# Optimization experiments

Measured on AMD Instinct MI355X. Metric: run time of the kernel, lower is better.

The kernel has to match this reference:

```python
import jax, jax.numpy as jnp
import numpy as np

N = 10000
D_IN = 512
D_OUT = 512
EDGE_P = 0.003  # ~30 avg degree


def setup_inputs() -> dict:
    key = jax.random.key(0)
    k_x, k_a, k_w1, k_b1, k_w2, k_b2 = jax.random.split(key, 6)
    x = jax.random.normal(k_x, (N, D_IN), dtype=jnp.float32)
    # sparse-ish binary adjacency, zero diagonal (GCNConv adds self-loops itself)
    adjacency = (jax.random.uniform(k_a, (N, N)) < EDGE_P).astype(jnp.float32)
    adjacency = adjacency * (1.0 - jnp.eye(N, dtype=jnp.float32))
    s1 = 1.0 / np.sqrt(D_IN)
    s2 = 1.0 / np.sqrt(D_OUT)
    W1 = jax.random.normal(k_w1, (D_IN, D_OUT), dtype=jnp.float32) * s1
    b1 = jax.random.normal(k_b1, (D_OUT,), dtype=jnp.float32) * 0.01
    W2 = jax.random.normal(k_w2, (D_OUT, D_OUT), dtype=jnp.float32) * s2
    b2 = jax.random.normal(k_b2, (D_OUT,), dtype=jnp.float32) * 0.01
    return {"x": x, "adjacency": adjacency, "W1": W1, "b1": b1, "W2": W2, "b2": b2}


def _gcn_norm(adjacency):
    # GCNConv gcn_norm: add self-loops (weight 1), deg = sum of incoming edge
    # weights at target (column sums), norm[i,j] = d_i^{-1/2} * Ahat[i,j] * d_j^{-1/2}
    n = adjacency.shape[0]
    Ahat = adjacency + jnp.eye(n, dtype=adjacency.dtype)
    deg = Ahat.sum(axis=0)
    dinv = jnp.where(deg > 0, deg ** -0.5, 0.0)
    return dinv[:, None] * Ahat * dinv[None, :]


def reference(x, adjacency, W1, b1, W2, b2):
    An = _gcn_norm(adjacency)  # [N, N]
    # out[j] = sum_i An[i,j] * (x W)[i]  ->  An.T @ (x W)
    h = jax.nn.relu(An.T @ (x @ W1) + b1)
    h = jax.nn.relu(An.T @ (h @ W2) + b2)
    return h
```

## Files before the change

kernel.cpp:

```cpp
#include <hip/hip_runtime.h>
#include <hip/hip_bf16.h>
#include <hip/hip_fp16.h>

#define N_NODES 10000
#define DFEAT 512
#define MPAD 10112
#define MAXDEG 96
#define NB_SPLITX 5056
#define NB_WSPLIT 512
#define GEMM_BLOCKS 316
#define NB_SCAN 10000

typedef __attribute__((ext_vector_type(8))) short short8x;
typedef __attribute__((ext_vector_type(4))) float f32x4;
typedef __attribute__((ext_vector_type(4))) _Float16 half4x;

__device__ __forceinline__ ushort f2bf(float f) {
    uint u = __builtin_bit_cast(uint, f);
    uint r = (u + 0x7FFFu + ((u >> 16) & 1u)) >> 16;
    return (ushort)r;
}
__device__ __forceinline__ float bf2f(ushort h) {
    uint u = ((uint)h) << 16;
    return __builtin_bit_cast(float, u);
}

typedef const __attribute__((address_space(1))) void gv_t;
typedef __attribute__((address_space(3))) void sv_t;
__device__ __forceinline__ void gload16(const void* g, void* l) {
    __builtin_amdgcn_global_load_lds((gv_t*)g, (sv_t*)l, 16, 0, 0);
}

__global__ __launch_bounds__(256) void prep_split(const float* __restrict__ X,
                                                  const float* __restrict__ W1,
                                                  const float* __restrict__ W2,
                                                  ushort* __restrict__ Ah,
                                                  ushort* __restrict__ Al,
                                                  ushort* __restrict__ W1hT,
                                                  ushort* __restrict__ W1lT,
                                                  ushort* __restrict__ W2hT,
                                                  ushort* __restrict__ W2lT) {
    const int bid = blockIdx.x;
    const int tid = threadIdx.x;
    if (bid < NB_SPLITX) {
        size_t idx = (size_t)bid * 256 + tid;
        int row = (int)(idx >> 7);
        float4 v = make_float4(0.f, 0.f, 0.f, 0.f);
        if (row < N_NODES) v = ((const float4*)X)[idx];
        ushort4 hi, lo;
        hi.x = f2bf(v.x); lo.x = f2bf(v.x - bf2f(hi.x));
        hi.y = f2bf(v.y); lo.y = f2bf(v.y - bf2f(hi.y));
        hi.z = f2bf(v.z); lo.z = f2bf(v.z - bf2f(hi.z));
        hi.w = f2bf(v.w); lo.w = f2bf(v.w - bf2f(hi.w));
        ((ushort4*)Ah)[idx] = hi;
        ((ushort4*)Al)[idx] = lo;
    } else {
        __shared__ float tile[32][33];
        int wb = bid - NB_SPLITX;
        const float* W = (wb < 256) ? W1 : W2;
        ushort* WhT = (wb < 256) ? W1hT : W2hT;
        ushort* WlT = (wb < 256) ? W1lT : W2lT;
        int wi = wb & 255;
        int n0 = (wi & 15) * 32, k0 = (wi >> 4) * 32;
        const int tx = tid & 31, ty = tid >> 5;
#pragma unroll
        for (int p = 0; p < 4; ++p)
            tile[ty + p * 8][tx] = W[(size_t)(k0 + ty + p * 8) * DFEAT + n0 + tx];
        __syncthreads();
#pragma unroll
        for (int p = 0; p < 4; ++p) {
            int n = n0 + ty + p * 8;
            int k = k0 + tx;
            float v = tile[tx][ty + p * 8];
            ushort h = f2bf(v);
            WhT[(size_t)n * DFEAT + k] = h;
            WlT[(size_t)n * DFEAT + k] = f2bf(v - bf2f(h));
        }
    }
}

template <bool PRE>
__device__ __forceinline__ void gemm_tile(const ushort* __restrict__ Ah,
                                          const ushort* __restrict__ Al,
                                          const ushort* __restrict__ BhT,
                                          const ushort* __restrict__ BlT,
                                          const int* __restrict__ cnt,
                                          _Float16* __restrict__ C, int M,
                                          int row0, int col0, int tid) {
    __shared__ ushort lAh[128 * 32];
    __shared__ ushort lAl[128 * 32];
    __shared__ ushort lBh[128 * 32];
    __shared__ ushort lBl[128 * 32];
    const int lane = tid & 63, wv = tid >> 6;
    const int wm = wv >> 1, wn = wv & 1;
    const int l15 = lane & 15, lg = lane >> 4;

    f32x4 acc[4][4];
#pragma unroll
    for (int i = 0; i < 4; ++i)
#pragma unroll
        for (int j = 0; j < 4; ++j) acc[i][j] = (f32x4){0.f, 0.f, 0.f, 0.f};

    for (int k0 = 0; k0 < 512; k0 += 32) {
#pragma unroll
        for (int c = 0; c < 2; ++c) {
            int o = (wv * 2 + c) * 1024 + lane * 16;
            int r = o >> 6;
            int gsl = ((o >> 4) & 3) ^ (r & 3);
            size_t ga = (size_t)(row0 + r) * 1024 + (size_t)(k0 * 2) + gsl * 16;
            size_t gb = (size_t)(col0 + r) * 1024 + (size_t)(k0 * 2) + gsl * 16;
            gload16((const char*)Ah + ga, (char*)lAh + o);
            gload16((const char*)Al + ga, (char*)lAl + o);
            gload16((const char*)BhT + gb, (char*)lBh + o);
            gload16((const char*)BlT + gb, (char*)lBl + o);
        }
        __syncthreads();

        short8x a_h[4], a_l[4], b_h[4], b_l[4];
#pragma unroll
        for (int i = 0; i < 4; ++i) {
            int r = wm * 64 + i * 16 + l15;
            int bo = r * 64 + ((lg ^ (r & 3)) << 4);
            a_h[i] = *(const short8x*)((const char*)lAh + bo);
            a_l[i] = *(const short8x*)((const char*)lAl + bo);
        }
#pragma unroll
        for (int j = 0; j < 4; ++j) {
            int n = wn * 64 + j * 16 + l15;
            int bo = n * 64 + ((lg ^ (n & 3)) << 4);
            b_h[j] = *(const short8x*)((const char*)lBh + bo);
            b_l[j] = *(const short8x*)((const char*)lBl + bo);
        }
#pragma unroll
        for (int i = 0; i < 4; ++i)
#pragma unroll
            for (int j = 0; j < 4; ++j) {
                acc[i][j] = __builtin_amdgcn_mfma_f32_16x16x32_bf16(a_h[i], b_h[j], acc[i][j], 0, 0, 0);
                acc[i][j] = __builtin_amdgcn_mfma_f32_16x16x32_bf16(a_h[i], b_l[j], acc[i][j], 0, 0, 0);
                acc[i][j] = __builtin_amdgcn_mfma_f32_16x16x32_bf16(a_l[i], b_h[j], acc[i][j], 0, 0, 0);
            }
        __syncthreads();
    }

#pragma unroll
    for (int i = 0; i < 4; ++i) {
#pragma unroll
        for (int r = 0; r < 4; ++r) {
            int grow = row0 + wm * 64 + i * 16 + lg * 4 + r;
            if (grow < M) {
                float dv = 1.0f;
                if (PRE) dv = 1.0f / sqrtf((float)cnt[grow] + 1.0f);
#pragma unroll
                for (int j = 0; j < 4; ++j) {
                    int gcol = col0 + wn * 64 + j * 16 + l15;
                    C[(size_t)grow * DFEAT + gcol] = (_Float16)(dv * acc[i][j][r]);
                }
            }
        }
    }
}

__global__ __launch_bounds__(256, 4) void mega_gemm_scan(const ushort* __restrict__ Ah,
                                                         const ushort* __restrict__ Al,
                                                         const ushort* __restrict__ BhT,
                                                         const ushort* __restrict__ BlT,
                                                         _Float16* __restrict__ C,
                                                         const float* __restrict__ A,
                                                         int* __restrict__ cursor,
                                                         int* __restrict__ slot) {
    const int bid = blockIdx.x;
    if (bid < GEMM_BLOCKS) {
        gemm_tile<false>(Ah, Al, BhT, BlT, nullptr, C, N_NODES,
                         (bid >> 2) * 128, (bid & 3) * 128, threadIdx.x);
    } else {
        const int row = bid - GEMM_BLOCKS;
        const int tid = threadIdx.x;
        const float4* Arow = (const float4*)(A + (size_t)row * N_NODES);
        float4 v[10];
#pragma unroll
        for (int q = 0; q < 9; ++q) v[q] = Arow[tid + q * 256];
        v[9] = (tid < 2500 - 2304) ? Arow[tid + 2304] : make_float4(0.f, 0.f, 0.f, 0.f);
#pragma unroll
        for (int q = 0; q < 10; ++q) {
            int c = tid + q * 256;
            float vv[4] = {v[q].x, v[q].y, v[q].z, v[q].w};
#pragma unroll
            for (int k = 0; k < 4; ++k) {
                if (vv[k] != 0.0f) {
                    int j = c * 4 + k;
                    int pos = atomicAdd(&cursor[j], 1);
                    if (pos < MAXDEG) slot[j * MAXDEG + pos] = row;
                }
            }
        }
    }
}

__global__ __launch_bounds__(256, 4) void gemm2(const ushort* __restrict__ Ah,
                                                const ushort* __restrict__ Al,
                                                const ushort* __restrict__ BhT,
                                                const ushort* __restrict__ BlT,
                                                const int* __restrict__ cursor,
                                                _Float16* __restrict__ C) {
    gemm_tile<true>(Ah, Al, BhT, BlT, cursor, C, N_NODES,
                    (blockIdx.x >> 2) * 128, (blockIdx.x & 3) * 128, threadIdx.x);
}

__global__ __launch_bounds__(128) void agg1(const _Float16* __restrict__ G,
                                            const int* __restrict__ cursor,
                                            const int* __restrict__ slot,
                                            const float* __restrict__ bias,
                                            ushort* __restrict__ Hh,
                                            ushort* __restrict__ Hl) {
    const int j = blockIdx.x;
    const int tid = threadIdx.x;
    __shared__ int sidx[MAXDEG];
    __shared__ float sw[MAXDEG];
    const half4x* G4 = (const half4x*)G;
    const int cj = cursor[j];
    const int cnt = min(cj, MAXDEG);
    if (tid < cnt) {
        int i = slot[j * MAXDEG + tid];
        sidx[tid] = i;
        sw[tid] = 1.0f / sqrtf((float)cursor[i] + 1.0f);
    }
    __syncthreads();
    const float dj = 1.0f / sqrtf((float)cj + 1.0f);
    half4x h = G4[(j << 7) + tid];
    float4 acc = make_float4(dj * (float)h[0], dj * (float)h[1],
                             dj * (float)h[2], dj * (float)h[3]);
    int c = 0;
    for (; c + 8 <= cnt; c += 8) {
        half4x u[8];
        float w[8];
#pragma unroll
        for (int q = 0; q < 8; ++q) { u[q] = G4[(sidx[c + q] << 7) + tid]; w[q] = sw[c + q]; }
#pragma unroll
        for (int q = 0; q < 8; ++q) {
            acc.x += w[q] * (float)u[q][0]; acc.y += w[q] * (float)u[q][1];
            acc.z += w[q] * (float)u[q][2]; acc.w += w[q] * (float)u[q][3];
        }
    }
    for (; c < cnt; ++c) {
        half4x u = G4[(sidx[c] << 7) + tid];
        float w = sw[c];
        acc.x += w * (float)u[0]; acc.y += w * (float)u[1];
        acc.z += w * (float)u[2]; acc.w += w * (float)u[3];
    }
    float4 b = ((const float4*)bias)[tid];
    float4 o;
    o.x = fmaxf(dj * acc.x + b.x, 0.0f);
    o.y = fmaxf(dj * acc.y + b.y, 0.0f);
    o.z = fmaxf(dj * acc.z + b.z, 0.0f);
    o.w = fmaxf(dj * acc.w + b.w, 0.0f);
    ushort4 hi, lo;
    hi.x = f2bf(o.x); lo.x = f2bf(o.x - bf2f(hi.x));
    hi.y = f2bf(o.y); lo.y = f2bf(o.y - bf2f(hi.y));
    hi.z = f2bf(o.z); lo.z = f2bf(o.z - bf2f(hi.z));
    hi.w = f2bf(o.w); lo.w = f2bf(o.w - bf2f(hi.w));
    ((ushort4*)(Hh + ((size_t)j << 9)))[tid] = hi;
    ((ushort4*)(Hl + ((size_t)j << 9)))[tid] = lo;
}

__global__ __launch_bounds__(128) void agg2(const _Float16* __restrict__ G,
                                            const int* __restrict__ cursor,
                                            const int* __restrict__ slot,
                                            const float* __restrict__ bias,
                                            float* __restrict__ out) {
    const int j = blockIdx.x;
    const int tid = threadIdx.x;
    __shared__ int sidx[MAXDEG];
    const half4x* G4 = (const half4x*)G;
    const int cj = cursor[j];
    const int cnt = min(cj, MAXDEG);
    if (tid < cnt) sidx[tid] = slot[j * MAXDEG + tid];
    __syncthreads();
    half4x h = G4[(j << 7) + tid];
    float4 acc = make_float4((float)h[0], (float)h[1], (float)h[2], (float)h[3]);
    int c = 0;
    for (; c + 8 <= cnt; c += 8) {
        half4x u[8];
#pragma unroll
        for (int q = 0; q < 8; ++q) u[q] = G4[(sidx[c + q] << 7) + tid];
#pragma unroll
        for (int q = 0; q < 8; ++q) {
            acc.x += (float)u[q][0]; acc.y += (float)u[q][1];
            acc.z += (float)u[q][2]; acc.w += (float)u[q][3];
        }
    }
    for (; c < cnt; ++c) {
        half4x u = G4[(sidx[c] << 7) + tid];
        acc.x += (float)u[0]; acc.y += (float)u[1];
        acc.z += (float)u[2]; acc.w += (float)u[3];
    }
    const float dj = 1.0f / sqrtf((float)cj + 1.0f);
    float4 b = ((const float4*)bias)[tid];
    float4 o;
    o.x = fmaxf(dj * acc.x + b.x, 0.0f);
    o.y = fmaxf(dj * acc.y + b.y, 0.0f);
    o.z = fmaxf(dj * acc.z + b.z, 0.0f);
    o.w = fmaxf(dj * acc.w + b.w, 0.0f);
    ((float4*)(out + ((size_t)j << 9)))[tid] = o;
}

extern "C" void kernel_launch(void* const* d_in, const int* in_sizes, int n_in,
                              void* d_out, int out_size, void* d_ws, size_t ws_size,
                              hipStream_t stream) {
    const float* x  = (const float*)d_in[0];
    const float* A  = (const float*)d_in[1];
    const float* W1 = (const float*)d_in[2];
    const float* b1 = (const float*)d_in[3];
    const float* W2 = (const float*)d_in[4];
    const float* b2 = (const float*)d_in[5];
    float* out = (float*)d_out;

    char* ws = (char*)d_ws;
    size_t off = 0;
    auto alloc = [&](size_t bytes) -> void* {
        void* p = ws + off;
        off = (off + bytes + 255) & ~(size_t)255;
        return p;
    };
    _Float16* XW16 = (_Float16*)alloc((size_t)MPAD * DFEAT * 2);
    ushort* Ah   = (ushort*)alloc((size_t)MPAD * DFEAT * 2);
    ushort* Al   = (ushort*)alloc((size_t)MPAD * DFEAT * 2);
    ushort* Hh   = (ushort*)alloc((size_t)MPAD * DFEAT * 2);
    ushort* Hl   = (ushort*)alloc((size_t)MPAD * DFEAT * 2);
    ushort* W1hT = (ushort*)alloc((size_t)DFEAT * DFEAT * 2);
    ushort* W1lT = (ushort*)alloc((size_t)DFEAT * DFEAT * 2);
    ushort* W2hT = (ushort*)alloc((size_t)DFEAT * DFEAT * 2);
    ushort* W2lT = (ushort*)alloc((size_t)DFEAT * DFEAT * 2);
    int*  cursor = (int*)alloc((size_t)N_NODES * 4);
    int*    slot = (int*)alloc((size_t)N_NODES * MAXDEG * 4);

    hipMemsetAsync(cursor, 0, (size_t)N_NODES * 4, stream);

    prep_split<<<NB_SPLITX + NB_WSPLIT, 256, 0, stream>>>(
        x, W1, W2, Ah, Al, W1hT, W1lT, W2hT, W2lT);

    mega_gemm_scan<<<GEMM_BLOCKS + NB_SCAN, 256, 0, stream>>>(
        Ah, Al, W1hT, W1lT, XW16, A, cursor, slot);

    agg1<<<N_NODES, 128, 0, stream>>>(XW16, cursor, slot, b1, Hh, Hl);

    gemm2<<<GEMM_BLOCKS, 256, 0, stream>>>(Hh, Hl, W2hT, W2lT, cursor, XW16);

    agg2<<<N_NODES, 128, 0, stream>>>(XW16, cursor, slot, b2, out);
}
```

Baseline: 658.2 us.

## Fuse bf16 hi/lo splitting of GEMM A operand into the GEMM tile load

The separate X split pass and the hi/lo outputs of agg1 are removed. The GEMMs now read fp32 activations directly and split them into bf16 hi/lo inside the tile loader, writing to swizzled LDS. The cursor memset is also folded into the weight-prep kernel, which saves a launch. The cost is that the A tile loads become synchronous register loads plus conversion ALU work, replacing the async global_load_lds path, and each tile's split is repeated by the 4 column blocks.

```diff
diff --git a/kernel.cpp b/kernel.cpp
--- a/kernel.cpp
+++ b/kernel.cpp
@@ -6,8 +6,8 @@
 #define DFEAT 512
 #define MPAD 10112
 #define MAXDEG 96
-#define NB_SPLITX 5056
 #define NB_WSPLIT 512
+#define NB_ZERO 40
 #define GEMM_BLOCKS 316
 #define NB_SCAN 10000
 
@@ -31,36 +31,21 @@
     __builtin_amdgcn_global_load_lds((gv_t*)g, (sv_t*)l, 16, 0, 0);
 }
 
-__global__ __launch_bounds__(256) void prep_split(const float* __restrict__ X,
-                                                  const float* __restrict__ W1,
-                                                  const float* __restrict__ W2,
-                                                  ushort* __restrict__ Ah,
-                                                  ushort* __restrict__ Al,
-                                                  ushort* __restrict__ W1hT,
-                                                  ushort* __restrict__ W1lT,
-                                                  ushort* __restrict__ W2hT,
-                                                  ushort* __restrict__ W2lT) {
+__global__ __launch_bounds__(256) void wprep(const float* __restrict__ W1,
+                                             const float* __restrict__ W2,
+                                             ushort* __restrict__ W1hT,
+                                             ushort* __restrict__ W1lT,
+                                             ushort* __restrict__ W2hT,
+                                             ushort* __restrict__ W2lT,
+                                             int* __restrict__ cursor) {
     const int bid = blockIdx.x;
     const int tid = threadIdx.x;
-    if (bid < NB_SPLITX) {
-        size_t idx = (size_t)bid * 256 + tid;
-        int row = (int)(idx >> 7);
-        float4 v = make_float4(0.f, 0.f, 0.f, 0.f);
-        if (row < N_NODES) v = ((const float4*)X)[idx];
-        ushort4 hi, lo;
-        hi.x = f2bf(v.x); lo.x = f2bf(v.x - bf2f(hi.x));
-        hi.y = f2bf(v.y); lo.y = f2bf(v.y - bf2f(hi.y));
-        hi.z = f2bf(v.z); lo.z = f2bf(v.z - bf2f(hi.z));
-        hi.w = f2bf(v.w); lo.w = f2bf(v.w - bf2f(hi.w));
-        ((ushort4*)Ah)[idx] = hi;
-        ((ushort4*)Al)[idx] = lo;
-    } else {
+    if (bid < NB_WSPLIT) {
         __shared__ float tile[32][33];
-        int wb = bid - NB_SPLITX;
-        const float* W = (wb < 256) ? W1 : W2;
-        ushort* WhT = (wb < 256) ? W1hT : W2hT;
-        ushort* WlT = (wb < 256) ? W1lT : W2lT;
-        int wi = wb & 255;
+        const float* W = (bid < 256) ? W1 : W2;
+        ushort* WhT = (bid < 256) ? W1hT : W2hT;
+        ushort* WlT = (bid < 256) ? W1lT : W2lT;
+        int wi = bid & 255;
         int n0 = (wi & 15) * 32, k0 = (wi >> 4) * 32;
         const int tx = tid & 31, ty = tid >> 5;
 #pragma unroll
@@ -76,12 +61,14 @@
             WhT[(size_t)n * DFEAT + k] = h;
             WlT[(size_t)n * DFEAT + k] = f2bf(v - bf2f(h));
         }
+    } else {
+        int j = (bid - NB_WSPLIT) * 256 + tid;
+        if (j < N_NODES) cursor[j] = 0;
     }
 }
 
 template <bool PRE>
-__device__ __forceinline__ void gemm_tile(const ushort* __restrict__ Ah,
-                                          const ushort* __restrict__ Al,
+__device__ __forceinline__ void gemm_tile(const float* __restrict__ Afp,
                                           const ushort* __restrict__ BhT,
                                           const ushort* __restrict__ BlT,
                                           const int* __restrict__ cnt,
@@ -107,12 +94,32 @@
             int o = (wv * 2 + c) * 1024 + lane * 16;
             int r = o >> 6;
             int gsl = ((o >> 4) & 3) ^ (r & 3);
-            size_t ga = (size_t)(row0 + r) * 1024 + (size_t)(k0 * 2) + gsl * 16;
             size_t gb = (size_t)(col0 + r) * 1024 + (size_t)(k0 * 2) + gsl * 16;
-            gload16((const char*)Ah + ga, (char*)lAh + o);
-            gload16((const char*)Al + ga, (char*)lAl + o);
             gload16((const char*)BhT + gb, (char*)lBh + o);
             gload16((const char*)BlT + gb, (char*)lBl + o);
+        }
+#pragma unroll
+        for (int c2 = 0; c2 < 2; ++c2) {
+            int t2 = tid + c2 * 256;
+            int r = t2 >> 2, sl = t2 & 3;
+            float4 v0 = make_float4(0.f, 0.f, 0.f, 0.f);
+            float4 v1 = make_float4(0.f, 0.f, 0.f, 0.f);
+            if (row0 + r < M) {
+                const float4* Xr = (const float4*)(Afp + (size_t)(row0 + r) * DFEAT + k0 + sl * 8);
+                v0 = Xr[0];
+                v1 = Xr[1];
+            }
+            float vv[8] = {v0.x, v0.y, v0.z, v0.w, v1.x, v1.y, v1.z, v1.w};
+            short8x hi, lo;
+#pragma unroll
+            for (int q = 0; q < 8; ++q) {
+                ushort h = f2bf(vv[q]);
+                hi[q] = (short)h;
+                lo[q] = (short)f2bf(vv[q] - bf2f(h));
+            }
+            int bo = r * 64 + ((sl ^ (r & 3)) << 4);
+            *(short8x*)((char*)lAh + bo) = hi;
+            *(short8x*)((char*)lAl + bo) = lo;
         }
         __syncthreads();
 
@@ -160,8 +167,7 @@
     }
 }
 
-__global__ __launch_bounds__(256, 4) void mega_gemm_scan(const ushort* __restrict__ Ah,
-                                                         const ushort* __restrict__ Al,
+__global__ __launch_bounds__(256, 4) void mega_gemm_scan(const float* __restrict__ X,
                                                          const ushort* __restrict__ BhT,
                                                          const ushort* __restrict__ BlT,
                                                          _Float16* __restrict__ C,
@@ -170,7 +176,7 @@
                                                          int* __restrict__ slot) {
     const int bid = blockIdx.x;
     if (bid < GEMM_BLOCKS) {
-        gemm_tile<false>(Ah, Al, BhT, BlT, nullptr, C, N_NODES,
+        gemm_tile<false>(X, BhT, BlT, nullptr, C, N_NODES,
                          (bid >> 2) * 128, (bid & 3) * 128, threadIdx.x);
     } else {
         const int row = bid - GEMM_BLOCKS;
@@ -196,13 +202,12 @@
     }
 }
 
-__global__ __launch_bounds__(256, 4) void gemm2(const ushort* __restrict__ Ah,
-                                                const ushort* __restrict__ Al,
+__global__ __launch_bounds__(256, 4) void gemm2(const float* __restrict__ H,
                                                 const ushort* __restrict__ BhT,
                                                 const ushort* __restrict__ BlT,
                                                 const int* __restrict__ cursor,
                                                 _Float16* __restrict__ C) {
-    gemm_tile<true>(Ah, Al, BhT, BlT, cursor, C, N_NODES,
+    gemm_tile<true>(H, BhT, BlT, cursor, C, N_NODES,
                     (blockIdx.x >> 2) * 128, (blockIdx.x & 3) * 128, threadIdx.x);
 }
 
@@ -210,8 +215,7 @@
                                             const int* __restrict__ cursor,
                                             const int* __restrict__ slot,
                                             const float* __restrict__ bias,
-                                            ushort* __restrict__ Hh,
-                                            ushort* __restrict__ Hl) {
+                                            float* __restrict__ H) {
     const int j = blockIdx.x;
     const int tid = threadIdx.x;
     __shared__ int sidx[MAXDEG];
@@ -253,13 +257,7 @@
     o.y = fmaxf(dj * acc.y + b.y, 0.0f);
     o.z = fmaxf(dj * acc.z + b.z, 0.0f);
     o.w = fmaxf(dj * acc.w + b.w, 0.0f);
-    ushort4 hi, lo;
-    hi.x = f2bf(o.x); lo.x = f2bf(o.x - bf2f(hi.x));
-    hi.y = f2bf(o.y); lo.y = f2bf(o.y - bf2f(hi.y));
-    hi.z = f2bf(o.z); lo.z = f2bf(o.z - bf2f(hi.z));
-    hi.w = f2bf(o.w); lo.w = f2bf(o.w - bf2f(hi.w));
-    ((ushort4*)(Hh + ((size_t)j << 9)))[tid] = hi;
-    ((ushort4*)(Hl + ((size_t)j << 9)))[tid] = lo;
+    ((float4*)(H + ((size_t)j << 9)))[tid] = o;
 }
 
 __global__ __launch_bounds__(128) void agg2(const _Float16* __restrict__ G,
@@ -322,10 +320,7 @@
         return p;
     };
     _Float16* XW16 = (_Float16*)alloc((size_t)MPAD * DFEAT * 2);
-    ushort* Ah   = (ushort*)alloc((size_t)MPAD * DFEAT * 2);
-    ushort* Al   = (ushort*)alloc((size_t)MPAD * DFEAT * 2);
-    ushort* Hh   = (ushort*)alloc((size_t)MPAD * DFEAT * 2);
-    ushort* Hl   = (ushort*)alloc((size_t)MPAD * DFEAT * 2);
+    float*  H    = (float*)alloc((size_t)MPAD * DFEAT * 4);
     ushort* W1hT = (ushort*)alloc((size_t)DFEAT * DFEAT * 2);
     ushort* W1lT = (ushort*)alloc((size_t)DFEAT * DFEAT * 2);
     ushort* W2hT = (ushort*)alloc((size_t)DFEAT * DFEAT * 2);
@@ -333,17 +328,14 @@
     int*  cursor = (int*)alloc((size_t)N_NODES * 4);
     int*    slot = (int*)alloc((size_t)N_NODES * MAXDEG * 4);
 
-    hipMemsetAsync(cursor, 0, (size_t)N_NODES * 4, stream);
-
-    prep_split<<<NB_SPLITX + NB_WSPLIT, 256, 0, stream>>>(
-        x, W1, W2, Ah, Al, W1hT, W1lT, W2hT, W2lT);
+    wprep<<<NB_WSPLIT + NB_ZERO, 256, 0, stream>>>(W1, W2, W1hT, W1lT, W2hT, W2lT, cursor);
 
     mega_gemm_scan<<<GEMM_BLOCKS + NB_SCAN, 256, 0, stream>>>(
-        Ah, Al, W1hT, W1lT, XW16, A, cursor, slot);
-
-    agg1<<<N_NODES, 128, 0, stream>>>(XW16, cursor, slot, b1, Hh, Hl);
-
-    gemm2<<<GEMM_BLOCKS, 256, 0, stream>>>(Hh, Hl, W2hT, W2lT, cursor, XW16);
+        x, W1hT, W1lT, XW16, A, cursor, slot);
+
+    agg1<<<N_NODES, 128, 0, stream>>>(XW16, cursor, slot, b1, H);
+
+    gemm2<<<GEMM_BLOCKS, 256, 0, stream>>>(H, W2hT, W2lT, cursor, XW16);
 
     agg2<<<N_NODES, 128, 0, stream>>>(XW16, cursor, slot, b2, out);
 }
```

New measurement: 657.1 us. About the same (-0.2%).
